# Kernel tuning notes

Measured on AMD Instinct MI355X. Metric: run time of the kernel, lower is better.

Reference implementation:

```python
import jax, jax.numpy as jnp
import numpy as np

SIGMA = 1.0

def setup_inputs() -> dict:
    key = jax.random.key(0)
    k1, k2 = jax.random.split(key)
    z = jax.random.normal(k1, (8192, 1024), dtype=jnp.float32)
    expert_keys = jax.random.normal(k2, (4096, 1024), dtype=jnp.float32)
    return {"z": z, "expert_keys": expert_keys}

def reference(z, expert_keys):
    # squared euclidean distances [N, E] = |z|^2 + |e|^2 - 2 z.e
    z_sq = jnp.sum(z * z, axis=-1, keepdims=True)          # [N, 1]
    e_sq = jnp.sum(expert_keys * expert_keys, axis=-1)     # [E]
    dist2 = z_sq + e_sq[None, :] - 2.0 * (z @ expert_keys.T)
    dist2 = jnp.maximum(dist2, 0.0)
    similarity = jnp.exp(-dist2 / (2.0 * SIGMA ** 2))       # [N, E]
    weights = jax.nn.softmax(similarity, axis=-1)            # [N, E]
    weighted_expert = weights @ expert_keys                  # [N, D]
    return (similarity, weighted_expert)
```

## Files before the change

### kernel.cpp

```cpp
#include <hip/hip_runtime.h>
#include <stdint.h>


#define M_TOK 8192
#define N_EXP 4096
#define D_DIM 1024

typedef __attribute__((ext_vector_type(4))) float f32x4;
typedef __attribute__((ext_vector_type(8))) short short8;
typedef unsigned short u16;
typedef unsigned int u32;

__device__ __forceinline__ u16 f32_to_bf16(float f) {
  u32 u = __builtin_bit_cast(u32, f);
  u += 0x7fff + ((u >> 16) & 1);
  return (u16)(u >> 16);
}

__device__ __forceinline__ void async16(const void* g, void* l) {
  __builtin_amdgcn_global_load_lds((__attribute__((address_space(1))) void*)(g),
                                   (__attribute__((address_space(3))) void*)(l),
                                   16, 0, 0);
}

__global__ __launch_bounds__(256) void prep_convert(const float* __restrict__ src,
                                                    u16* __restrict__ dst,
                                                    float* __restrict__ sq) {
  int row = blockIdx.x;
  int t = threadIdx.x;
  const float4 v = ((const float4*)(src + (size_t)row * D_DIM))[t];
  ushort4 h;
  h.x = f32_to_bf16(v.x); h.y = f32_to_bf16(v.y);
  h.z = f32_to_bf16(v.z); h.w = f32_to_bf16(v.w);
  ((ushort4*)(dst + (size_t)row * D_DIM))[t] = h;
  float p = v.x * v.x + v.y * v.y + v.z * v.z + v.w * v.w;
#pragma unroll
  for (int off = 1; off < 64; off <<= 1) p += __shfl_xor(p, off, 64);
  __shared__ float partial[4];
  if ((t & 63) == 0) partial[t >> 6] = p;
  __syncthreads();
  if (t == 0) sq[row] = partial[0] + partial[1] + partial[2] + partial[3];
}

__global__ __launch_bounds__(256) void transpose_bf16(const u16* __restrict__ src,
                                                      u16* __restrict__ dst) {
  __shared__ u16 tile[64][65];
  int e0 = blockIdx.x * 64;
  int d0 = blockIdx.y * 64;
  int t = threadIdx.x;
  int lr = t >> 4;
  int lc = (t & 15) * 4;
#pragma unroll
  for (int r8 = 0; r8 < 4; ++r8) {
    int row = lr + r8 * 16;
    ushort4 v = *(const ushort4*)(src + (size_t)(e0 + row) * D_DIM + d0 + lc);
    tile[row][lc + 0] = v.x; tile[row][lc + 1] = v.y;
    tile[row][lc + 2] = v.z; tile[row][lc + 3] = v.w;
  }
  __syncthreads();
#pragma unroll
  for (int r8 = 0; r8 < 4; ++r8) {
    int dl = lr + r8 * 16;
    ushort4 v;
    v.x = tile[lc + 0][dl]; v.y = tile[lc + 1][dl];
    v.z = tile[lc + 2][dl]; v.w = tile[lc + 3][dl];
    *(ushort4*)(dst + (size_t)(d0 + dl) * N_EXP + e0 + lc) = v;
  }
}

template <int EPI>
__global__ __launch_bounds__(256) void gemm_bt(const u16* __restrict__ A,
                                               const u16* __restrict__ Bt,
                                               int Mdim, int Ndim, int Kdim,
                                               float* __restrict__ out, int ldo,
                                               const float* __restrict__ a_sq,
                                               const float* __restrict__ b_sq,
                                               float* __restrict__ rowsum,
                                               u16* __restrict__ wb,
                                               const float* __restrict__ scale) {
  constexpr int BM = 128, BN = 128, BK = 64;
  __shared__ __align__(16) u16 smA[BM * BK];
  __shared__ __align__(16) u16 smB[BN * BK];

  const int nTilesN = Ndim / BN;
  const int nwg = (Mdim / BM) * nTilesN;
  const int cpx = nwg >> 3;
  const int wg = blockIdx.x;
  const int swz = (wg & 7) * cpx + (wg >> 3);
  const int m0 = (swz / nTilesN) * BM;
  const int n0 = (swz % nTilesN) * BN;

  const int t = threadIdx.x;
  const int l = t & 63;
  const int w = t >> 6;
  const int wr = w >> 1, wc = w & 1;

  const int lr8 = l >> 3;
  const int cswz = (((l & 7) ^ lr8) << 3);

  f32x4 acc[4][4];
#pragma unroll
  for (int i = 0; i < 4; ++i)
#pragma unroll
    for (int j = 0; j < 4; ++j) acc[i][j] = (f32x4){0.f, 0.f, 0.f, 0.f};

  for (int k0 = 0; k0 < Kdim; k0 += BK) {
    __syncthreads();
#pragma unroll
    for (int i = 0; i < 4; ++i) {
      int s = i * 4 + w;
      int row = s * 8 + lr8;
      async16(A + (size_t)(m0 + row) * Kdim + k0 + cswz, smA + s * 512);
    }
#pragma unroll
    for (int i = 0; i < 4; ++i) {
      int s = i * 4 + w;
      int row = s * 8 + lr8;
      async16(Bt + (size_t)(n0 + row) * Kdim + k0 + cswz, smB + s * 512);
    }
    __syncthreads();

#pragma unroll
    for (int ks = 0; ks < 2; ++ks) {
      short8 af[4], bf[4];
      const int lrow = l & 15;
      const int kb = ks * 64 + ((l >> 4) << 4);
#pragma unroll
      for (int mi = 0; mi < 4; ++mi) {
        int row = wr * 64 + mi * 16 + lrow;
        int addr = row * 128 + (kb ^ ((row & 7) << 4));
        af[mi] = *(const short8*)(smA + (addr >> 1));
      }
#pragma unroll
      for (int ni = 0; ni < 4; ++ni) {
        int row = wc * 64 + ni * 16 + lrow;
        int addr = row * 128 + (kb ^ ((row & 7) << 4));
        bf[ni] = *(const short8*)(smB + (addr >> 1));
      }
#pragma unroll
      for (int mi = 0; mi < 4; ++mi)
#pragma unroll
        for (int ni = 0; ni < 4; ++ni)
          acc[mi][ni] = __builtin_amdgcn_mfma_f32_16x16x32_bf16(
              bf[ni], af[mi], acc[mi][ni], 0, 0, 0);
    }
  }

  const int lcol = l & 15;
  const int rgrp = l >> 4;
  if (EPI == 1) {
#pragma unroll
    for (int mi = 0; mi < 4; ++mi) {
      int grow = m0 + wr * 64 + mi * 16 + lcol;
      float zq = a_sq[grow];
      float esum = 0.f;
#pragma unroll
      for (int ni = 0; ni < 4; ++ni) {
        int ncol = n0 + wc * 64 + ni * 16 + rgrp * 4;
        f32x4 simv;
        ushort4 wv;
#pragma unroll
        for (int r = 0; r < 4; ++r) {
          float eq = b_sq[ncol + r];
          float dist2 = fmaxf(zq + eq - 2.0f * acc[mi][ni][r], 0.0f);
          float sim = __expf(-0.5f * dist2);
          simv[r] = sim;
          float es = __expf(sim);
          (&wv.x)[r] = f32_to_bf16(es);
          esum += es;
        }
        __builtin_nontemporal_store(simv, (f32x4*)(out + (size_t)grow * ldo + ncol));
        if (wb) *(ushort4*)(wb + (size_t)grow * ldo + ncol) = wv;
      }
      esum += __shfl_xor(esum, 16, 64);
      esum += __shfl_xor(esum, 32, 64);
      if (rgrp == 0) atomicAdd(&rowsum[grow], esum);
    }
  } else {
#pragma unroll
    for (int mi = 0; mi < 4; ++mi) {
      int grow = m0 + wr * 64 + mi * 16 + lcol;
      float s = scale ? (1.0f / scale[grow]) : 1.0f;
#pragma unroll
      for (int ni = 0; ni < 4; ++ni) {
        int ncol = n0 + wc * 64 + ni * 16 + rgrp * 4;
        f32x4 v = acc[mi][ni] * s;
        *(f32x4*)(out + (size_t)grow * ldo + ncol) = v;
      }
    }
  }
}

__global__ __launch_bounds__(256) void weights_kernel(const float* __restrict__ sim,
                                                      const float* __restrict__ rowsum,
                                                      u16* __restrict__ wb) {
  size_t i = ((size_t)blockIdx.x * 256 + threadIdx.x) * 8;
  int row = (int)(i >> 12);
  float inv = 1.0f / rowsum[row];
  float4 a = *(const float4*)(sim + i);
  float4 b = *(const float4*)(sim + i + 4);
  u32 w0 = (u32)f32_to_bf16(__expf(a.x) * inv) | ((u32)f32_to_bf16(__expf(a.y) * inv) << 16);
  u32 w1 = (u32)f32_to_bf16(__expf(a.z) * inv) | ((u32)f32_to_bf16(__expf(a.w) * inv) << 16);
  u32 w2 = (u32)f32_to_bf16(__expf(b.x) * inv) | ((u32)f32_to_bf16(__expf(b.y) * inv) << 16);
  u32 w3 = (u32)f32_to_bf16(__expf(b.z) * inv) | ((u32)f32_to_bf16(__expf(b.w) * inv) << 16);
  uint4 o; o.x = w0; o.y = w1; o.z = w2; o.w = w3;
  *(uint4*)(wb + i) = o;
}

extern "C" void kernel_launch(void* const* d_in, const int* in_sizes, int n_in,
                              void* d_out, int out_size, void* d_ws, size_t ws_size,
                              hipStream_t stream) {
  const float* z = (const float*)d_in[0];
  const float* e = (const float*)d_in[1];
  float* out = (float*)d_out;
  float* sim = out;
  float* wout = out + (size_t)M_TOK * N_EXP;

  char* ws = (char*)d_ws;
  const size_t MB = (size_t)1 << 20;
  const bool fused = ws_size >= 96 * MB + 80 * 1024;

  if (fused) {
    u16* zb  = (u16*)ws;
    u16* eb  = (u16*)(ws + 16 * MB);
    u16* ebT = (u16*)(ws + 24 * MB);
    u16* Wb  = (u16*)(ws + 32 * MB);
    float* z_sq   = (float*)(ws + 96 * MB);
    float* e_sq   = (float*)(ws + 96 * MB + 32768);
    float* rowsum = (float*)(ws + 96 * MB + 49152);

    prep_convert<<<M_TOK, 256, 0, stream>>>(z, zb, z_sq);
    prep_convert<<<N_EXP, 256, 0, stream>>>(e, eb, e_sq);
    transpose_bf16<<<dim3(N_EXP / 64, D_DIM / 64), 256, 0, stream>>>(eb, ebT);
    (void)hipMemsetAsync(rowsum, 0, M_TOK * sizeof(float), stream);

    gemm_bt<1><<<(M_TOK / 128) * (N_EXP / 128), 256, 0, stream>>>(
        zb, eb, M_TOK, N_EXP, D_DIM, sim, N_EXP, z_sq, e_sq, rowsum, Wb, nullptr);

    gemm_bt<0><<<(M_TOK / 128) * (D_DIM / 128), 256, 0, stream>>>(
        Wb, ebT, M_TOK, D_DIM, N_EXP, wout, D_DIM, nullptr, nullptr, nullptr,
        nullptr, rowsum);
  } else {
    u16* Wb  = (u16*)ws;
    u16* zb  = (u16*)ws;
    u16* eb  = (u16*)(ws + 64 * MB);
    u16* ebT = (u16*)(ws + 72 * MB);
    float* z_sq   = (float*)(ws + 80 * MB);
    float* e_sq   = (float*)(ws + 80 * MB + 32768);
    float* rowsum = (float*)(ws + 80 * MB + 49152);

    prep_convert<<<M_TOK, 256, 0, stream>>>(z, zb, z_sq);
    prep_convert<<<N_EXP, 256, 0, stream>>>(e, eb, e_sq);
    transpose_bf16<<<dim3(N_EXP / 64, D_DIM / 64), 256, 0, stream>>>(eb, ebT);
    (void)hipMemsetAsync(rowsum, 0, M_TOK * sizeof(float), stream);

    gemm_bt<1><<<(M_TOK / 128) * (N_EXP / 128), 256, 0, stream>>>(
        zb, eb, M_TOK, N_EXP, D_DIM, sim, N_EXP, z_sq, e_sq, rowsum, nullptr, nullptr);

    weights_kernel<<<(M_TOK * (size_t)N_EXP) / (8 * 256), 256, 0, stream>>>(sim, rowsum, Wb);

    gemm_bt<0><<<(M_TOK / 128) * (D_DIM / 128), 256, 0, stream>>>(
        Wb, ebT, M_TOK, D_DIM, N_EXP, wout, D_DIM, nullptr, nullptr, nullptr,
        nullptr, nullptr);
  }
}
```

Before: 211.6 us.

## Double-buffer GEMM LDS tiles and merge prep conversion launches

The GEMM main loop now keeps two LDS buffers and issues the async global-to-LDS loads for the next K tile before computing on the current one, with one barrier per iteration instead of two. This aims to hide global load latency behind the MFMA work. LDS use doubles to 64 KB per block, which may reduce occupancy. The two prep_convert launches are merged into one grid, the e_sq loads in the epilogue are vectorised, and the similarity store becomes a regular store instead of a nontemporal one.

Result: faster. 201.1 us (-5.0%).

```diff
diff --git a/kernel.cpp b/kernel.cpp
--- a/kernel.cpp
+++ b/kernel.cpp
@@ -23,23 +23,39 @@
                                    16, 0, 0);
 }
 
-__global__ __launch_bounds__(256) void prep_convert(const float* __restrict__ src,
-                                                    u16* __restrict__ dst,
-                                                    float* __restrict__ sq) {
+__global__ __launch_bounds__(256) void prep_convert2(const float* __restrict__ zsrc,
+                                                     const float* __restrict__ esrc,
+                                                     u16* __restrict__ zdst,
+                                                     u16* __restrict__ edst,
+                                                     float* __restrict__ zsq,
+                                                     float* __restrict__ esq) {
   int row = blockIdx.x;
+  const float* src;
+  u16* dst;
+  float* sq;
+  if (row < M_TOK) {
+    src = zsrc + (size_t)row * D_DIM;
+    dst = zdst + (size_t)row * D_DIM;
+    sq = zsq + row;
+  } else {
+    int r = row - M_TOK;
+    src = esrc + (size_t)r * D_DIM;
+    dst = edst + (size_t)r * D_DIM;
+    sq = esq + r;
+  }
   int t = threadIdx.x;
-  const float4 v = ((const float4*)(src + (size_t)row * D_DIM))[t];
+  const float4 v = ((const float4*)src)[t];
   ushort4 h;
   h.x = f32_to_bf16(v.x); h.y = f32_to_bf16(v.y);
   h.z = f32_to_bf16(v.z); h.w = f32_to_bf16(v.w);
-  ((ushort4*)(dst + (size_t)row * D_DIM))[t] = h;
+  ((ushort4*)dst)[t] = h;
   float p = v.x * v.x + v.y * v.y + v.z * v.z + v.w * v.w;
 #pragma unroll
   for (int off = 1; off < 64; off <<= 1) p += __shfl_xor(p, off, 64);
   __shared__ float partial[4];
   if ((t & 63) == 0) partial[t >> 6] = p;
   __syncthreads();
-  if (t == 0) sq[row] = partial[0] + partial[1] + partial[2] + partial[3];
+  if (t == 0) *sq = partial[0] + partial[1] + partial[2] + partial[3];
 }
 
 __global__ __launch_bounds__(256) void transpose_bf16(const u16* __restrict__ src,
@@ -79,8 +95,8 @@
                                                u16* __restrict__ wb,
                                                const float* __restrict__ scale) {
   constexpr int BM = 128, BN = 128, BK = 64;
-  __shared__ __align__(16) u16 smA[BM * BK];
-  __shared__ __align__(16) u16 smB[BN * BK];
+  __shared__ __align__(16) u16 smA[2 * BM * BK];
+  __shared__ __align__(16) u16 smB[2 * BN * BK];
 
   const int nTilesN = Ndim / BN;
   const int nwg = (Mdim / BM) * nTilesN;
@@ -104,22 +120,32 @@
 #pragma unroll
     for (int j = 0; j < 4; ++j) acc[i][j] = (f32x4){0.f, 0.f, 0.f, 0.f};
 
-  for (int k0 = 0; k0 < Kdim; k0 += BK) {
-    __syncthreads();
-#pragma unroll
-    for (int i = 0; i < 4; ++i) {
-      int s = i * 4 + w;
-      int row = s * 8 + lr8;
-      async16(A + (size_t)(m0 + row) * Kdim + k0 + cswz, smA + s * 512);
-    }
-#pragma unroll
-    for (int i = 0; i < 4; ++i) {
-      int s = i * 4 + w;
-      int row = s * 8 + lr8;
-      async16(Bt + (size_t)(n0 + row) * Kdim + k0 + cswz, smB + s * 512);
-    }
-    __syncthreads();
-
+  const int nIter = Kdim / BK;
+
+#pragma unroll
+  for (int i = 0; i < 4; ++i) {
+    int s = i * 4 + w;
+    int row = s * 8 + lr8;
+    async16(A + (size_t)(m0 + row) * Kdim + cswz, smA + s * 512);
+    async16(Bt + (size_t)(n0 + row) * Kdim + cswz, smB + s * 512);
+  }
+  __syncthreads();
+
+  int cur = 0;
+  for (int it = 0; it < nIter; ++it) {
+    if (it + 1 < nIter) {
+      const int k0 = (it + 1) * BK;
+      const int nb = (cur ^ 1) * 8192;
+#pragma unroll
+      for (int i = 0; i < 4; ++i) {
+        int s = i * 4 + w;
+        int row = s * 8 + lr8;
+        async16(A + (size_t)(m0 + row) * Kdim + k0 + cswz, smA + nb + s * 512);
+        async16(Bt + (size_t)(n0 + row) * Kdim + k0 + cswz, smB + nb + s * 512);
+      }
+    }
+
+    const int cbase = cur * 8192;
 #pragma unroll
     for (int ks = 0; ks < 2; ++ks) {
       short8 af[4], bf[4];
@@ -129,13 +155,13 @@
       for (int mi = 0; mi < 4; ++mi) {
         int row = wr * 64 + mi * 16 + lrow;
         int addr = row * 128 + (kb ^ ((row & 7) << 4));
-        af[mi] = *(const short8*)(smA + (addr >> 1));
+        af[mi] = *(const short8*)(smA + cbase + (addr >> 1));
       }
 #pragma unroll
       for (int ni = 0; ni < 4; ++ni) {
         int row = wc * 64 + ni * 16 + lrow;
         int addr = row * 128 + (kb ^ ((row & 7) << 4));
-        bf[ni] = *(const short8*)(smB + (addr >> 1));
+        bf[ni] = *(const short8*)(smB + cbase + (addr >> 1));
       }
 #pragma unroll
       for (int mi = 0; mi < 4; ++mi)
@@ -144,6 +170,9 @@
           acc[mi][ni] = __builtin_amdgcn_mfma_f32_16x16x32_bf16(
               bf[ni], af[mi], acc[mi][ni], 0, 0, 0);
     }
+
+    __syncthreads();
+    cur ^= 1;
   }
 
   const int lcol = l & 15;
@@ -157,19 +186,19 @@
 #pragma unroll
       for (int ni = 0; ni < 4; ++ni) {
         int ncol = n0 + wc * 64 + ni * 16 + rgrp * 4;
+        f32x4 eqv = *(const f32x4*)(b_sq + ncol);
         f32x4 simv;
         ushort4 wv;
 #pragma unroll
         for (int r = 0; r < 4; ++r) {
-          float eq = b_sq[ncol + r];
-          float dist2 = fmaxf(zq + eq - 2.0f * acc[mi][ni][r], 0.0f);
+          float dist2 = fmaxf(zq + eqv[r] - 2.0f * acc[mi][ni][r], 0.0f);
           float sim = __expf(-0.5f * dist2);
           simv[r] = sim;
           float es = __expf(sim);
           (&wv.x)[r] = f32_to_bf16(es);
           esum += es;
         }
-        __builtin_nontemporal_store(simv, (f32x4*)(out + (size_t)grow * ldo + ncol));
+        *(f32x4*)(out + (size_t)grow * ldo + ncol) = simv;
         if (wb) *(ushort4*)(wb + (size_t)grow * ldo + ncol) = wv;
       }
       esum += __shfl_xor(esum, 16, 64);
@@ -229,8 +258,7 @@
     float* e_sq   = (float*)(ws + 96 * MB + 32768);
     float* rowsum = (float*)(ws + 96 * MB + 49152);
 
-    prep_convert<<<M_TOK, 256, 0, stream>>>(z, zb, z_sq);
-    prep_convert<<<N_EXP, 256, 0, stream>>>(e, eb, e_sq);
+    prep_convert2<<<M_TOK + N_EXP, 256, 0, stream>>>(z, e, zb, eb, z_sq, e_sq);
     transpose_bf16<<<dim3(N_EXP / 64, D_DIM / 64), 256, 0, stream>>>(eb, ebT);
     (void)hipMemsetAsync(rowsum, 0, M_TOK * sizeof(float), stream);
 
@@ -249,8 +277,7 @@
     float* e_sq   = (float*)(ws + 80 * MB + 32768);
     float* rowsum = (float*)(ws + 80 * MB + 49152);
 
-    prep_convert<<<M_TOK, 256, 0, stream>>>(z, zb, z_sq);
-    prep_convert<<<N_EXP, 256, 0, stream>>>(e, eb, e_sq);
+    prep_convert2<<<M_TOK + N_EXP, 256, 0, stream>>>(z, e, zb, eb, z_sq, e_sq);
     transpose_bf16<<<dim3(N_EXP / 64, D_DIM / 64), 256, 0, stream>>>(eb, ebT);
     (void)hipMemsetAsync(rowsum, 0, M_TOK * sizeof(float), stream);
 
```
